# Kernel tuning notes

Measured on AMD Instinct MI355X. Metric: run time of the kernel, lower is better.

The kernel has to match this reference:

```python
import jax, jax.numpy as jnp
import numpy as np

N = 20000
NUM_FEATURES = 128
HIDDEN = 32
HEADS = 8
NUM_CLASSES = 40
NEG_SLOPE = 0.2  # PyG GATConv default


def setup_inputs() -> dict:
    key = jax.random.key(0)
    ks = jax.random.split(key, 10)
    E = 640000
    x = jax.random.normal(ks[0], (N, NUM_FEATURES), dtype=jnp.float32)
    edge_index = jax.random.randint(ks[1], (2, E), 0, N, dtype=jnp.int64)
    s1 = 1.0 / np.sqrt(NUM_FEATURES)
    s2 = 1.0 / np.sqrt(HIDDEN * HEADS)
    W1 = jax.random.normal(ks[2], (NUM_FEATURES, HEADS * HIDDEN), dtype=jnp.float32) * s1
    a1_src = jax.random.normal(ks[3], (HEADS, HIDDEN), dtype=jnp.float32) * s2
    a1_dst = jax.random.normal(ks[4], (HEADS, HIDDEN), dtype=jnp.float32) * s2
    b1 = jnp.zeros((HEADS * HIDDEN,), dtype=jnp.float32)
    W2 = jax.random.normal(ks[5], (HEADS * HIDDEN, NUM_CLASSES), dtype=jnp.float32) * s2
    a2_src = jax.random.normal(ks[6], (1, NUM_CLASSES), dtype=jnp.float32) * 0.1
    a2_dst = jax.random.normal(ks[7], (1, NUM_CLASSES), dtype=jnp.float32) * 0.1
    b2 = jnp.zeros((NUM_CLASSES,), dtype=jnp.float32)
    return {"x": x, "edge_index": edge_index, "W1": W1, "a1_src": a1_src,
            "a1_dst": a1_dst, "b1": b1, "W2": W2, "a2_src": a2_src,
            "a2_dst": a2_dst, "b2": b2}


def gat_conv(x, src, dst, W, a_src, a_dst, bias, heads, out_ch, concat):
    """PyG GATConv (eval mode, self-loops already appended to src/dst)."""
    n = x.shape[0]
    h = (x @ W).reshape(n, heads, out_ch)                     # [N,H,C]
    alpha_s = jnp.einsum('nhc,hc->nh', h, a_src)              # [N,H]
    alpha_d = jnp.einsum('nhc,hc->nh', h, a_dst)
    e = alpha_s[src] + alpha_d[dst]                           # [E,H]
    e = jax.nn.leaky_relu(e, NEG_SLOPE)
    # segment softmax over incoming edges of each destination node
    m = jax.ops.segment_max(e, dst, num_segments=n)           # [N,H]
    m = jax.lax.stop_gradient(m)
    ex = jnp.exp(e - m[dst])                                  # [E,H]
    denom = jax.ops.segment_sum(ex, dst, num_segments=n)      # [N,H]
    alpha = ex / denom[dst]                                   # [E,H]
    msg = alpha[:, :, None] * h[src]                          # [E,H,C]
    out = jax.ops.segment_sum(msg, dst, num_segments=n)       # [N,H,C]
    if concat:
        out = out.reshape(n, heads * out_ch)
    else:
        out = out.mean(axis=1)
    return out + bias


def reference(x, edge_index, W1, a1_src, a1_dst, b1, W2, a2_src, a2_dst, b2):
    loops = jnp.arange(N, dtype=edge_index.dtype)
    src = jnp.concatenate([edge_index[0], loops])
    dst = jnp.concatenate([edge_index[1], loops])
    h = gat_conv(x, src, dst, W1, a1_src, a1_dst, b1, HEADS, HIDDEN, True)
    h = jax.nn.elu(h)
    out = gat_conv(h, src, dst, W2, a2_src, a2_dst, b2, 1, NUM_CLASSES, False)
    return jax.nn.log_softmax(out, axis=1)
```

## Files before the change

kernel.cpp:

```cpp
#include <hip/hip_runtime.h>
#include <hip/hip_fp16.h>
#include <math.h>

#define N 20000
#define F 128
#define C1 256
#define HEADS 8
#define HID 32
#define NC 40
#define NCP 64
#define NEG 0.2f

#define BSHIFT 7
#define NB 157
#define HBLOCKS 256
#define HM (NB * HBLOCKS)

#define PREPW_BLOCKS 16
#define W2PW_BLOCKS 6

#define QS ((size_t)N * 64)

typedef _Float16 half8 __attribute__((ext_vector_type(8)));
typedef float f32x4 __attribute__((ext_vector_type(4)));

__device__ __forceinline__ int edge_stride(const int* ei) {
    return (ei[1] == 0 && ei[3] == 0 && ei[5] == 0 && ei[7] == 0 && ei[9] == 0) ? 2 : 1;
}

__device__ __forceinline__ float lrelu(float v) { return v > 0.f ? v : NEG * v; }

__global__ __launch_bounds__(256) void k_misc(
    const float* __restrict__ W1, _Float16* __restrict__ w1sw,
    const float* __restrict__ W2, _Float16* __restrict__ w2sw,
    const int* __restrict__ ei, int E, int* __restrict__ hist)
{
    const int b = blockIdx.x;
    const int tid = threadIdx.x;
    if (b < PREPW_BLOCKS) {
        const int slot = b * 256 + tid;
        const int lane = slot & 63;
        const int tile = slot >> 6;
        const int nt = tile & 15, ks = tile >> 4;
        const int n = nt * 16 + (lane & 15);
        const int k0 = ks * 32 + (lane >> 4) * 8;
        half8 tmp;
#pragma unroll
        for (int j = 0; j < 8; j++) tmp[j] = (_Float16)W1[(k0 + j) * C1 + n];
        *reinterpret_cast<half8*>(&w1sw[(size_t)slot * 8]) = tmp;
    } else if (b < PREPW_BLOCKS + W2PW_BLOCKS) {
        const int slot = (b - PREPW_BLOCKS) * 256 + tid;
        const int lane = slot & 63;
        const int f = slot >> 6;
        const int nt = f % 3, ks = f / 3;
        const int n = nt * 16 + (lane & 15);
        const int k0 = ks * 32 + (lane >> 4) * 8;
        half8 tmp;
#pragma unroll
        for (int j = 0; j < 8; j++)
            tmp[j] = (n < NC) ? (_Float16)W2[(k0 + j) * NC + n] : (_Float16)0.f;
        *reinterpret_cast<half8*>(&w2sw[(size_t)slot * 8]) = tmp;
    } else {
        __shared__ int hcnt[NB];
        const int hb = b - PREPW_BLOCKS - W2PW_BLOCKS;
        if (tid < NB) hcnt[tid] = 0;
        __syncthreads();
        const int ET = E + N;
        const int per = (ET + HBLOCKS - 1) / HBLOCKS;
        const int lo = hb * per;
        const int hi = (lo + per < ET) ? (lo + per) : ET;
        const int st = edge_stride(ei);
        for (int i = lo + tid; i < hi; i += 256) {
            const int d = (i < E) ? ei[(size_t)st * (E + i)] : (i - E);
            atomicAdd(&hcnt[d >> BSHIFT], 1);
        }
        __syncthreads();
        if (tid < NB) hist[tid * HBLOCKS + hb] = hcnt[tid];
    }
}

__global__ __launch_bounds__(256) void k_gemm1_mfma(
    const float* __restrict__ x, const _Float16* __restrict__ w1sw,
    const float* __restrict__ a1s, const float* __restrict__ a1d,
    __half* __restrict__ qh1,
    float* __restrict__ as1, float* __restrict__ ad1)
{
    const int lane = threadIdx.x & 63;
    const int wid = (blockIdx.x * 256 + threadIdx.x) >> 6;
    const int m0 = wid * 16;
    const int g = lane >> 4, lm = lane & 15;
    const int arow = m0 + lm;
    half8 a[4];
    if (arow < N) {
        const float* xr = x + (size_t)arow * F;
#pragma unroll
        for (int ks = 0; ks < 4; ks++) {
            const float4 v0 = *reinterpret_cast<const float4*>(&xr[ks * 32 + g * 8]);
            const float4 v1 = *reinterpret_cast<const float4*>(&xr[ks * 32 + g * 8 + 4]);
            half8 t;
            t[0] = (_Float16)v0.x; t[1] = (_Float16)v0.y; t[2] = (_Float16)v0.z; t[3] = (_Float16)v0.w;
            t[4] = (_Float16)v1.x; t[5] = (_Float16)v1.y; t[6] = (_Float16)v1.z; t[7] = (_Float16)v1.w;
            a[ks] = t;
        }
    } else {
#pragma unroll
        for (int ks = 0; ks < 4; ks++) {
            half8 t;
#pragma unroll
            for (int j = 0; j < 8; j++) t[j] = (_Float16)0.f;
            a[ks] = t;
        }
    }
    const int rbase = m0 + g * 4;
    float ps[4] = {0.f, 0.f, 0.f, 0.f}, pd[4] = {0.f, 0.f, 0.f, 0.f};
#pragma unroll
    for (int nt = 0; nt < 16; nt++) {
        f32x4 acc = {0.f, 0.f, 0.f, 0.f};
#pragma unroll
        for (int ks = 0; ks < 4; ks++) {
            const half8 bfr = *reinterpret_cast<const half8*>(&w1sw[(size_t)((ks * 16 + nt) * 64 + lane) * 8]);
            acc = __builtin_amdgcn_mfma_f32_16x16x32_f16(a[ks], bfr, acc, 0, 0, 0);
        }
        const int col = nt * 16 + lm;
        const int q = col >> 6, cq = col & 63;
        const float av = a1s[col], dv = a1d[col];
#pragma unroll
        for (int r = 0; r < 4; r++) {
            const int row = rbase + r;
            if (row < N) qh1[(size_t)q * QS + (size_t)row * 64 + cq] = __float2half((float)acc[r]);
            ps[r] = fmaf((float)acc[r], av, ps[r]);
            pd[r] = fmaf((float)acc[r], dv, pd[r]);
        }
        if (nt & 1) {
#pragma unroll
            for (int off = 1; off <= 8; off <<= 1) {
#pragma unroll
                for (int r = 0; r < 4; r++) {
                    ps[r] += __shfl_xor(ps[r], off);
                    pd[r] += __shfl_xor(pd[r], off);
                }
            }
            if (lm == 0) {
                const int head = nt >> 1;
#pragma unroll
                for (int r = 0; r < 4; r++) {
                    const int row = rbase + r;
                    if (row < N) {
                        as1[row * HEADS + head] = ps[r];
                        ad1[row * HEADS + head] = pd[r];
                    }
                }
            }
#pragma unroll
            for (int r = 0; r < 4; r++) { ps[r] = 0.f; pd[r] = 0.f; }
        }
    }
}

__global__ __launch_bounds__(256) void k_scatter2(
    const int* __restrict__ ei, int E, const int* __restrict__ hist,
    int* __restrict__ buck, int* __restrict__ bstart)
{
    __shared__ int cur[NB];
    __shared__ int bs[160];
    __shared__ int wbase[4];
    const int hb = blockIdx.x;
    const int tid = threadIdx.x;
    const int lane = tid & 63, wid = tid >> 6;
    int rp = 0;
    if (tid < NB) {
        const int4* hp = (const int4*)&hist[tid * HBLOCKS];
        int s = 0;
#pragma unroll 4
        for (int k = 0; k < 64; k++) {
            const int4 v = hp[k];
            s += (v.x + v.y) + (v.z + v.w);
            const int b4 = 4 * k;
            rp += ((b4 + 0) < hb ? v.x : 0) + ((b4 + 1) < hb ? v.y : 0)
                + ((b4 + 2) < hb ? v.z : 0) + ((b4 + 3) < hb ? v.w : 0);
        }
        bs[tid] = s;
    }
    __syncthreads();
    const int vin = (tid < NB) ? bs[tid] : 0;
    int v = vin;
#pragma unroll
    for (int off = 1; off < 64; off <<= 1) {
        const int u = __shfl_up(v, off, 64);
        if (lane >= off) v += u;
    }
    if (lane == 63) wbase[wid] = v;
    __syncthreads();
    if (tid < 64) {
        int w = (lane < 4) ? wbase[lane] : 0;
        const int orig = w;
#pragma unroll
        for (int off = 1; off < 4; off <<= 1) {
            const int u = __shfl_up(w, off, 64);
            if (lane >= off) w += u;
        }
        if (lane < 4) wbase[lane] = w - orig;
    }
    __syncthreads();
    if (tid < NB) {
        const int base = wbase[wid] + v - vin;
        cur[tid] = base + rp;
        if (hb == 0) bstart[tid] = base;
    }
    __syncthreads();
    const int ET = E + N;
    const int per = (ET + HBLOCKS - 1) / HBLOCKS;
    const int lo = hb * per;
    const int hi = (lo + per < ET) ? (lo + per) : ET;
    const int st = edge_stride(ei);
    for (int i = lo + tid; i < hi; i += 256) {
        int s, d;
        if (i < E) { s = ei[(size_t)st * i]; d = ei[(size_t)st * (E + i)]; }
        else       { s = i - E; d = i - E; }
        const int slot = atomicAdd(&cur[d >> BSHIFT], 1);
        buck[slot] = ((d & 127) << 16) | s;
    }
}

__global__ __launch_bounds__(256) void k_bucket(
    const int* __restrict__ bstart, const int* __restrict__ buck, int ET,
    int* __restrict__ csr, int* __restrict__ rowptr)
{
    __shared__ int cnt[128];
    __shared__ int pfx[128];
    const int b = blockIdx.x;
    const int tid = threadIdx.x;
    const int start = bstart[b];
    const int end = (b == NB - 1) ? ET : bstart[b + 1];
    if (tid < 128) cnt[tid] = 0;
    __syncthreads();
    for (int i = start + tid; i < end; i += 256)
        atomicAdd(&cnt[buck[i] >> 16], 1);
    __syncthreads();
    if (tid < 128) pfx[tid] = cnt[tid];
    __syncthreads();
    for (int off = 1; off < 128; off <<= 1) {
        int u = 0;
        if (tid < 128 && tid >= off) u = pfx[tid - off];
        __syncthreads();
        if (tid < 128) pfx[tid] += u;
        __syncthreads();
    }
    if (tid < 128) {
        const int node = b * 128 + tid;
        const int ebase = start + pfx[tid] - cnt[tid];
        if (node < N) rowptr[node] = ebase;
        cnt[tid] = ebase;
    }
    if (b == NB - 1 && tid == 0) rowptr[N] = ET;
    if (b == NB - 1 && tid < 64) csr[ET + tid] = 0;
    __syncthreads();
    for (int i = start + tid; i < end; i += 256) {
        const int val = buck[i];
        const int slot = atomicAdd(&cnt[val >> 16], 1);
        csr[slot] = val & 0xFFFF;
    }
}

__global__ __launch_bounds__(256) void k_agg1(
    const int* __restrict__ rowptr, const int* __restrict__ csr,
    const __half* __restrict__ qh1,
    const float* __restrict__ as1, const float* __restrict__ ad1,
    const float* __restrict__ b1, __half* __restrict__ h1p)
{
    __shared__ __align__(16) float wlds[8][2][36];
    __shared__ __align__(16) int slds[8][36];
    const int tid = threadIdx.x;
    const int l5 = tid & 31;
    const int sub = tid >> 5;
    const int hq = blockIdx.x & 3;
    const int n = (blockIdx.x >> 2) * 8 + sub;
    const int cq = l5 * 2;
    const int hsel = l5 >> 4;
    const float2 dv2 = *reinterpret_cast<const float2*>(&ad1[n * HEADS + hq * 2]);
    const int beg = rowptr[n], end = rowptr[n + 1];
    const __half* plane = qh1 + (size_t)hq * QS;
    float* w0 = wlds[sub][0];
    float* w1 = wlds[sub][1];
    const float* wc = wlds[sub][hsel];
    int* sl = slds[sub];
    float ax = 0.f, ay = 0.f, accw = 0.f;
    for (int cs = beg; cs < end; cs += 32) {
        const int m = end - cs;
        {
            const int s = csr[cs + l5];
            const float2 a2 = *reinterpret_cast<const float2*>(&as1[s * HEADS + hq * 2]);
            const bool ok = l5 < m;
            sl[l5] = s;
            w0[l5] = ok ? __expf(lrelu(a2.x + dv2.x)) : 0.f;
            w1[l5] = ok ? __expf(lrelu(a2.y + dv2.y)) : 0.f;
        }
        const int mm8 = (m < 32) ? ((m + 7) & ~7) : 32;
        for (int j0 = 0; j0 < mm8; j0 += 8) {
            const int4 sa = *reinterpret_cast<const int4*>(&sl[j0]);
            const int4 sb = *reinterpret_cast<const int4*>(&sl[j0 + 4]);
            const float4 wa = *reinterpret_cast<const float4*>(&wc[j0]);
            const float4 wb = *reinterpret_cast<const float4*>(&wc[j0 + 4]);
            const float2 gA = __half22float2(*reinterpret_cast<const __half2*>(&plane[(size_t)sa.x * 64 + cq]));
            const float2 gB = __half22float2(*reinterpret_cast<const __half2*>(&plane[(size_t)sa.y * 64 + cq]));
            const float2 gC = __half22float2(*reinterpret_cast<const __half2*>(&plane[(size_t)sa.z * 64 + cq]));
            const float2 gD = __half22float2(*reinterpret_cast<const __half2*>(&plane[(size_t)sa.w * 64 + cq]));
            const float2 gE = __half22float2(*reinterpret_cast<const __half2*>(&plane[(size_t)sb.x * 64 + cq]));
            const float2 gF = __half22float2(*reinterpret_cast<const __half2*>(&plane[(size_t)sb.y * 64 + cq]));
            const float2 gG = __half22float2(*reinterpret_cast<const __half2*>(&plane[(size_t)sb.z * 64 + cq]));
            const float2 gH = __half22float2(*reinterpret_cast<const __half2*>(&plane[(size_t)sb.w * 64 + cq]));
            accw += (wa.x + wa.y) + (wa.z + wa.w) + (wb.x + wb.y) + (wb.z + wb.w);
            ax = fmaf(wa.x, gA.x, ax); ay = fmaf(wa.x, gA.y, ay);
            ax = fmaf(wa.y, gB.x, ax); ay = fmaf(wa.y, gB.y, ay);
            ax = fmaf(wa.z, gC.x, ax); ay = fmaf(wa.z, gC.y, ay);
            ax = fmaf(wa.w, gD.x, ax); ay = fmaf(wa.w, gD.y, ay);
            ax = fmaf(wb.x, gE.x, ax); ay = fmaf(wb.x, gE.y, ay);
            ax = fmaf(wb.y, gF.x, ax); ay = fmaf(wb.y, gF.y, ay);
            ax = fmaf(wb.z, gG.x, ax); ay = fmaf(wb.z, gG.y, ay);
            ax = fmaf(wb.w, gH.x, ax); ay = fmaf(wb.w, gH.y, ay);
        }
    }
    const float inv = 1.f / accw;
    const int ch = hq * 64 + cq;
    float ox = ax * inv + b1[ch];
    float oy = ay * inv + b1[ch + 1];
    ox = (ox > 0.f) ? ox : (__expf(ox) - 1.f);
    oy = (oy > 0.f) ? oy : (__expf(oy) - 1.f);
    *reinterpret_cast<__half2*>(&h1p[(size_t)n * C1 + ch]) = __floats2half2_rn(ox, oy);
}

__global__ __launch_bounds__(256) void k_gemm2_mfma(
    const __half* __restrict__ h1p, const _Float16* __restrict__ w2sw,
    const float* __restrict__ a2s, const float* __restrict__ a2d,
    __half* __restrict__ h2h, float* __restrict__ as2, float* __restrict__ ad2)
{
    const int lane = threadIdx.x & 63;
    const int wid = (blockIdx.x * 256 + threadIdx.x) >> 6;
    const int m0 = wid * 16;
    const int g = lane >> 4, lm = lane & 15;
    const int arow = m0 + lm;
    half8 a[8];
    if (arow < N) {
        const __half* hr = h1p + (size_t)arow * C1;
#pragma unroll
        for (int ks = 0; ks < 8; ks++)
            a[ks] = *reinterpret_cast<const half8*>(&hr[ks * 32 + g * 8]);
    } else {
#pragma unroll
        for (int ks = 0; ks < 8; ks++) {
            half8 t;
#pragma unroll
            for (int j = 0; j < 8; j++) t[j] = (_Float16)0.f;
            a[ks] = t;
        }
    }
    f32x4 acc[3];
#pragma unroll
    for (int nt = 0; nt < 3; nt++) acc[nt] = (f32x4){0.f, 0.f, 0.f, 0.f};
#pragma unroll
    for (int ks = 0; ks < 8; ks++) {
#pragma unroll
        for (int nt = 0; nt < 3; nt++) {
            const half8 bfr = *reinterpret_cast<const half8*>(&w2sw[(size_t)((ks * 3 + nt) * 64 + lane) * 8]);
            acc[nt] = __builtin_amdgcn_mfma_f32_16x16x32_f16(a[ks], bfr, acc[nt], 0, 0, 0);
        }
    }
    const int rbase = m0 + g * 4;
    float av[3], dvv[3];
#pragma unroll
    for (int nt = 0; nt < 3; nt++) {
        const int col = nt * 16 + lm;
        av[nt]  = (col < NC) ? a2s[col] : 0.f;
        dvv[nt] = (col < NC) ? a2d[col] : 0.f;
    }
#pragma unroll
    for (int r = 0; r < 4; r++) {
        const int row = rbase + r;
        float ps = 0.f, pd = 0.f;
#pragma unroll
        for (int nt = 0; nt < 3; nt++) {
            const float v = (float)acc[nt][r];
            const int col = nt * 16 + lm;
            if (row < N && col < NC) h2h[(size_t)row * NCP + col] = __float2half(v);
            ps = fmaf(v, av[nt], ps);
            pd = fmaf(v, dvv[nt], pd);
        }
#pragma unroll
        for (int off = 1; off <= 8; off <<= 1) {
            ps += __shfl_xor(ps, off);
            pd += __shfl_xor(pd, off);
        }
        if (lm == 0 && row < N) { as2[row] = ps; ad2[row] = pd; }
    }
}

__global__ __launch_bounds__(256) void k_agg2(
    const int* __restrict__ rowptr, const int* __restrict__ csr,
    const __half* __restrict__ h2h, const float* __restrict__ as2,
    const float* __restrict__ ad2, const float* __restrict__ b2,
    float* __restrict__ out)
{
    __shared__ __align__(16) float wl[4][68];
    __shared__ __align__(16) int sl2[4][68];
    const int lane = threadIdx.x & 63;
    const int wv = threadIdx.x >> 6;
    const int n = (blockIdx.x * blockDim.x + threadIdx.x) >> 6;
    const int c = lane;
    const int cc = (c < NC) ? c : (NC - 1);
    const float adv = ad2[n];
    const int beg = rowptr[n], end = rowptr[n + 1];
    float* w = wl[wv];
    int* sl = sl2[wv];
    float acc = 0.f, accw = 0.f;
    for (int cs = beg; cs < end; cs += 64) {
        const int m = end - cs;
        {
            const int s = csr[cs + lane];
            sl[lane] = s;
            w[lane] = (lane < m) ? __expf(lrelu(as2[s] + adv)) : 0.f;
        }
        const int mm8 = (m < 64) ? ((m + 7) & ~7) : 64;
        for (int j0 = 0; j0 < mm8; j0 += 8) {
            const int4 sa = *reinterpret_cast<const int4*>(&sl[j0]);
            const int4 sb = *reinterpret_cast<const int4*>(&sl[j0 + 4]);
            const float4 wa = *reinterpret_cast<const float4*>(&w[j0]);
            const float4 wb = *reinterpret_cast<const float4*>(&w[j0 + 4]);
            const float g0 = __half2float(h2h[(size_t)sa.x * NCP + cc]);
            const float g1 = __half2float(h2h[(size_t)sa.y * NCP + cc]);
            const float g2 = __half2float(h2h[(size_t)sa.z * NCP + cc]);
            const float g3 = __half2float(h2h[(size_t)sa.w * NCP + cc]);
            const float g4 = __half2float(h2h[(size_t)sb.x * NCP + cc]);
            const float g5 = __half2float(h2h[(size_t)sb.y * NCP + cc]);
            const float g6 = __half2float(h2h[(size_t)sb.z * NCP + cc]);
            const float g7 = __half2float(h2h[(size_t)sb.w * NCP + cc]);
            accw += (wa.x + wa.y) + (wa.z + wa.w) + (wb.x + wb.y) + (wb.z + wb.w);
            acc = fmaf(wa.x, g0, acc);
            acc = fmaf(wa.y, g1, acc);
            acc = fmaf(wa.z, g2, acc);
            acc = fmaf(wa.w, g3, acc);
            acc = fmaf(wb.x, g4, acc);
            acc = fmaf(wb.y, g5, acc);
            acc = fmaf(wb.z, g6, acc);
            acc = fmaf(wb.w, g7, acc);
        }
    }
    const float v = acc / accw + b2[cc];
    float m = (c < NC) ? v : -1e30f;
#pragma unroll
    for (int off = 32; off >= 1; off >>= 1) m = fmaxf(m, __shfl_xor(m, off));
    float S = (c < NC) ? __expf(v - m) : 0.f;
#pragma unroll
    for (int off = 32; off >= 1; off >>= 1) S += __shfl_xor(S, off);
    if (c < NC) out[(size_t)n * NC + c] = v - m - logf(S);
}

extern "C" void kernel_launch(void* const* d_in, const int* in_sizes, int n_in,
                              void* d_out, int out_size, void* d_ws, size_t ws_size,
                              hipStream_t stream)
{
    const float* x   = (const float*)d_in[0];
    const int*   ei  = (const int*)d_in[1];
    const float* W1  = (const float*)d_in[2];
    const float* a1s = (const float*)d_in[3];
    const float* a1d = (const float*)d_in[4];
    const float* b1  = (const float*)d_in[5];
    const float* W2  = (const float*)d_in[6];
    const float* a2s = (const float*)d_in[7];
    const float* a2d = (const float*)d_in[8];
    const float* b2  = (const float*)d_in[9];
    float* out = (float*)d_out;

    const int E  = in_sizes[1] / 2;
    const int ET = E + N;

    auto align64 = [](size_t v) { return (v + 63) & ~(size_t)63; };
    char* ws = (char*)d_ws;
    size_t off = 0;
    _Float16* w1sw = (_Float16*)(ws + off); off = align64(off + (size_t)4096 * 8 * 2);
    _Float16* w2sw = (_Float16*)(ws + off); off = align64(off + (size_t)1536 * 8 * 2);
    __half* qh1 = (__half*)(ws + off); off = align64(off + (size_t)N * C1 * 2);
    __half* h1p = (__half*)(ws + off); off = align64(off + (size_t)N * C1 * 2);
    __half* h2h = (__half*)(ws + off); off = align64(off + (size_t)N * NCP * 2);
    float* as1 = (float*)(ws + off); off = align64(off + (size_t)N * HEADS * 4);
    float* ad1 = (float*)(ws + off); off = align64(off + (size_t)N * HEADS * 4);
    float* as2 = (float*)(ws + off); off = align64(off + (size_t)N * 4);
    float* ad2 = (float*)(ws + off); off = align64(off + (size_t)N * 4);
    int* hist   = (int*)(ws + off); off = align64(off + (size_t)HM * 4);
    int* bstart = (int*)(ws + off); off = align64(off + (size_t)NB * 4);
    int* buck   = (int*)(ws + off); off = align64(off + (size_t)ET * 4);
    int* rowptr = (int*)(ws + off); off = align64(off + (size_t)(N + 1) * 4);
    int* csr    = (int*)(ws + off); off = align64(off + (size_t)ET * 4 + 256);

    k_misc<<<PREPW_BLOCKS + W2PW_BLOCKS + HBLOCKS, 256, 0, stream>>>(W1, w1sw, W2, w2sw, ei, E, hist);
    k_gemm1_mfma<<<313, 256, 0, stream>>>(x, w1sw, a1s, a1d, qh1, as1, ad1);
    k_scatter2<<<HBLOCKS, 256, 0, stream>>>(ei, E, hist, buck, bstart);
    k_bucket<<<NB, 256, 0, stream>>>(bstart, buck, ET, csr, rowptr);
    k_agg1<<<N / 2, 256, 0, stream>>>(rowptr, csr, qh1, as1, ad1, b1, h1p);
    k_gemm2_mfma<<<313, 256, 0, stream>>>(h1p, w2sw, a2s, a2d, h2h, as2, ad2);
    k_agg2<<<5000, 256, 0, stream>>>(rowptr, csr, h2h, as2, ad2, b2, out);
}
```

Measured before the change: 183.4 us.

## Split GEMM1 columns across waves, persistent agg1 grid, prefetch next edge chunk

GEMM1 now gives each wave half of the 16 output column tiles, doubling the grid to 626 blocks for more parallelism. The agg1 kernel switches from one block per 8 nodes to a fixed 2048-block grid-stride loop, and both aggregation kernels prefetch the next chunk's source indices and attention scores while the current chunk is processed. The aim is to hide gather latency and cut launch and tail costs. In exchange, each GEMM1 wave reloads the full A fragment to do half the work, and the persistent loop may balance load less evenly.

```diff
diff --git a/kernel.cpp b/kernel.cpp
--- a/kernel.cpp
+++ b/kernel.cpp
@@ -20,6 +20,7 @@
 #define W2PW_BLOCKS 6
 
 #define QS ((size_t)N * 64)
+#define AGG1_BLOCKS 2048
 
 typedef _Float16 half8 __attribute__((ext_vector_type(8)));
 typedef float f32x4 __attribute__((ext_vector_type(4)));
@@ -87,7 +88,9 @@
 {
     const int lane = threadIdx.x & 63;
     const int wid = (blockIdx.x * 256 + threadIdx.x) >> 6;
-    const int m0 = wid * 16;
+    const int tile = wid >> 1;
+    const int hs = wid & 1;
+    const int m0 = tile * 16;
     const int g = lane >> 4, lm = lane & 15;
     const int arow = m0 + lm;
     half8 a[4];
@@ -114,7 +117,8 @@
     const int rbase = m0 + g * 4;
     float ps[4] = {0.f, 0.f, 0.f, 0.f}, pd[4] = {0.f, 0.f, 0.f, 0.f};
 #pragma unroll
-    for (int nt = 0; nt < 16; nt++) {
+    for (int ntl = 0; ntl < 8; ntl++) {
+        const int nt = hs * 8 + ntl;
         f32x4 acc = {0.f, 0.f, 0.f, 0.f};
 #pragma unroll
         for (int ks = 0; ks < 4; ks++) {
@@ -131,7 +135,7 @@
             ps[r] = fmaf((float)acc[r], av, ps[r]);
             pd[r] = fmaf((float)acc[r], dv, pd[r]);
         }
-        if (nt & 1) {
+        if (ntl & 1) {
 #pragma unroll
             for (int off = 1; off <= 8; off <<= 1) {
 #pragma unroll
@@ -141,7 +145,7 @@
                 }
             }
             if (lm == 0) {
-                const int head = nt >> 1;
+                const int head = hs * 4 + (ntl >> 1);
 #pragma unroll
                 for (int r = 0; r < 4; r++) {
                     const int row = rbase + r;
@@ -274,59 +278,67 @@
     const int l5 = tid & 31;
     const int sub = tid >> 5;
     const int hq = blockIdx.x & 3;
-    const int n = (blockIdx.x >> 2) * 8 + sub;
+    const int slotsPerQ = (gridDim.x >> 2) * 8;
+    const int slot0 = (blockIdx.x >> 2) * 8 + sub;
     const int cq = l5 * 2;
     const int hsel = l5 >> 4;
-    const float2 dv2 = *reinterpret_cast<const float2*>(&ad1[n * HEADS + hq * 2]);
-    const int beg = rowptr[n], end = rowptr[n + 1];
     const __half* plane = qh1 + (size_t)hq * QS;
     float* w0 = wlds[sub][0];
     float* w1 = wlds[sub][1];
     const float* wc = wlds[sub][hsel];
     int* sl = slds[sub];
-    float ax = 0.f, ay = 0.f, accw = 0.f;
-    for (int cs = beg; cs < end; cs += 32) {
-        const int m = end - cs;
-        {
-            const int s = csr[cs + l5];
-            const float2 a2 = *reinterpret_cast<const float2*>(&as1[s * HEADS + hq * 2]);
-            const bool ok = l5 < m;
-            sl[l5] = s;
-            w0[l5] = ok ? __expf(lrelu(a2.x + dv2.x)) : 0.f;
-            w1[l5] = ok ? __expf(lrelu(a2.y + dv2.y)) : 0.f;
-        }
-        const int mm8 = (m < 32) ? ((m + 7) & ~7) : 32;
-        for (int j0 = 0; j0 < mm8; j0 += 8) {
-            const int4 sa = *reinterpret_cast<const int4*>(&sl[j0]);
-            const int4 sb = *reinterpret_cast<const int4*>(&sl[j0 + 4]);
-            const float4 wa = *reinterpret_cast<const float4*>(&wc[j0]);
-            const float4 wb = *reinterpret_cast<const float4*>(&wc[j0 + 4]);
-            const float2 gA = __half22float2(*reinterpret_cast<const __half2*>(&plane[(size_t)sa.x * 64 + cq]));
-            const float2 gB = __half22float2(*reinterpret_cast<const __half2*>(&plane[(size_t)sa.y * 64 + cq]));
-            const float2 gC = __half22float2(*reinterpret_cast<const __half2*>(&plane[(size_t)sa.z * 64 + cq]));
-            const float2 gD = __half22float2(*reinterpret_cast<const __half2*>(&plane[(size_t)sa.w * 64 + cq]));
-            const float2 gE = __half22float2(*reinterpret_cast<const __half2*>(&plane[(size_t)sb.x * 64 + cq]));
-            const float2 gF = __half22float2(*reinterpret_cast<const __half2*>(&plane[(size_t)sb.y * 64 + cq]));
-            const float2 gG = __half22float2(*reinterpret_cast<const __half2*>(&plane[(size_t)sb.z * 64 + cq]));
-            const float2 gH = __half22float2(*reinterpret_cast<const __half2*>(&plane[(size_t)sb.w * 64 + cq]));
-            accw += (wa.x + wa.y) + (wa.z + wa.w) + (wb.x + wb.y) + (wb.z + wb.w);
-            ax = fmaf(wa.x, gA.x, ax); ay = fmaf(wa.x, gA.y, ay);
-            ax = fmaf(wa.y, gB.x, ax); ay = fmaf(wa.y, gB.y, ay);
-            ax = fmaf(wa.z, gC.x, ax); ay = fmaf(wa.z, gC.y, ay);
-            ax = fmaf(wa.w, gD.x, ax); ay = fmaf(wa.w, gD.y, ay);
-            ax = fmaf(wb.x, gE.x, ax); ay = fmaf(wb.x, gE.y, ay);
-            ax = fmaf(wb.y, gF.x, ax); ay = fmaf(wb.y, gF.y, ay);
-            ax = fmaf(wb.z, gG.x, ax); ay = fmaf(wb.z, gG.y, ay);
-            ax = fmaf(wb.w, gH.x, ax); ay = fmaf(wb.w, gH.y, ay);
-        }
-    }
-    const float inv = 1.f / accw;
     const int ch = hq * 64 + cq;
-    float ox = ax * inv + b1[ch];
-    float oy = ay * inv + b1[ch + 1];
-    ox = (ox > 0.f) ? ox : (__expf(ox) - 1.f);
-    oy = (oy > 0.f) ? oy : (__expf(oy) - 1.f);
-    *reinterpret_cast<__half2*>(&h1p[(size_t)n * C1 + ch]) = __floats2half2_rn(ox, oy);
+    const float bx = b1[ch], by = b1[ch + 1];
+    for (int n = slot0; n < N; n += slotsPerQ) {
+        const float2 dv2 = *reinterpret_cast<const float2*>(&ad1[n * HEADS + hq * 2]);
+        const int beg = rowptr[n], end = rowptr[n + 1];
+        float ax = 0.f, ay = 0.f, accw = 0.f;
+        int s_pf = csr[beg + l5];
+        float2 a_pf = *reinterpret_cast<const float2*>(&as1[s_pf * HEADS + hq * 2]);
+        for (int cs = beg; cs < end; cs += 32) {
+            const int m = end - cs;
+            {
+                const bool ok = l5 < m;
+                sl[l5] = s_pf;
+                w0[l5] = ok ? __expf(lrelu(a_pf.x + dv2.x)) : 0.f;
+                w1[l5] = ok ? __expf(lrelu(a_pf.y + dv2.y)) : 0.f;
+            }
+            if (cs + 32 < end) {
+                s_pf = csr[cs + 32 + l5];
+                a_pf = *reinterpret_cast<const float2*>(&as1[s_pf * HEADS + hq * 2]);
+            }
+            const int mm8 = (m < 32) ? ((m + 7) & ~7) : 32;
+            for (int j0 = 0; j0 < mm8; j0 += 8) {
+                const int4 sa = *reinterpret_cast<const int4*>(&sl[j0]);
+                const int4 sb = *reinterpret_cast<const int4*>(&sl[j0 + 4]);
+                const float4 wa = *reinterpret_cast<const float4*>(&wc[j0]);
+                const float4 wb = *reinterpret_cast<const float4*>(&wc[j0 + 4]);
+                const float2 gA = __half22float2(*reinterpret_cast<const __half2*>(&plane[(size_t)sa.x * 64 + cq]));
+                const float2 gB = __half22float2(*reinterpret_cast<const __half2*>(&plane[(size_t)sa.y * 64 + cq]));
+                const float2 gC = __half22float2(*reinterpret_cast<const __half2*>(&plane[(size_t)sa.z * 64 + cq]));
+                const float2 gD = __half22float2(*reinterpret_cast<const __half2*>(&plane[(size_t)sa.w * 64 + cq]));
+                const float2 gE = __half22float2(*reinterpret_cast<const __half2*>(&plane[(size_t)sb.x * 64 + cq]));
+                const float2 gF = __half22float2(*reinterpret_cast<const __half2*>(&plane[(size_t)sb.y * 64 + cq]));
+                const float2 gG = __half22float2(*reinterpret_cast<const __half2*>(&plane[(size_t)sb.z * 64 + cq]));
+                const float2 gH = __half22float2(*reinterpret_cast<const __half2*>(&plane[(size_t)sb.w * 64 + cq]));
+                accw += (wa.x + wa.y) + (wa.z + wa.w) + (wb.x + wb.y) + (wb.z + wb.w);
+                ax = fmaf(wa.x, gA.x, ax); ay = fmaf(wa.x, gA.y, ay);
+                ax = fmaf(wa.y, gB.x, ax); ay = fmaf(wa.y, gB.y, ay);
+                ax = fmaf(wa.z, gC.x, ax); ay = fmaf(wa.z, gC.y, ay);
+                ax = fmaf(wa.w, gD.x, ax); ay = fmaf(wa.w, gD.y, ay);
+                ax = fmaf(wb.x, gE.x, ax); ay = fmaf(wb.x, gE.y, ay);
+                ax = fmaf(wb.y, gF.x, ax); ay = fmaf(wb.y, gF.y, ay);
+                ax = fmaf(wb.z, gG.x, ax); ay = fmaf(wb.z, gG.y, ay);
+                ax = fmaf(wb.w, gH.x, ax); ay = fmaf(wb.w, gH.y, ay);
+            }
+        }
+        const float inv = 1.f / accw;
+        float ox = ax * inv + bx;
+        float oy = ay * inv + by;
+        ox = (ox > 0.f) ? ox : (__expf(ox) - 1.f);
+        oy = (oy > 0.f) ? oy : (__expf(oy) - 1.f);
+        *reinterpret_cast<__half2*>(&h1p[(size_t)n * C1 + ch]) = __floats2half2_rn(ox, oy);
+    }
 }
 
 __global__ __launch_bounds__(256) void k_gemm2_mfma(
@@ -412,12 +424,17 @@
     float* w = wl[wv];
     int* sl = sl2[wv];
     float acc = 0.f, accw = 0.f;
+    int s_pf = csr[beg + lane];
+    float a_pf = as2[s_pf];
     for (int cs = beg; cs < end; cs += 64) {
         const int m = end - cs;
         {
-            const int s = csr[cs + lane];
-            sl[lane] = s;
-            w[lane] = (lane < m) ? __expf(lrelu(as2[s] + adv)) : 0.f;
+            sl[lane] = s_pf;
+            w[lane] = (lane < m) ? __expf(lrelu(a_pf + adv)) : 0.f;
+        }
+        if (cs + 64 < end) {
+            s_pf = csr[cs + 64 + lane];
+            a_pf = as2[s_pf];
         }
         const int mm8 = (m < 64) ? ((m + 7) & ~7) : 64;
         for (int j0 = 0; j0 < mm8; j0 += 8) {
@@ -492,10 +509,10 @@
     int* csr    = (int*)(ws + off); off = align64(off + (size_t)ET * 4 + 256);
 
     k_misc<<<PREPW_BLOCKS + W2PW_BLOCKS + HBLOCKS, 256, 0, stream>>>(W1, w1sw, W2, w2sw, ei, E, hist);
-    k_gemm1_mfma<<<313, 256, 0, stream>>>(x, w1sw, a1s, a1d, qh1, as1, ad1);
+    k_gemm1_mfma<<<626, 256, 0, stream>>>(x, w1sw, a1s, a1d, qh1, as1, ad1);
     k_scatter2<<<HBLOCKS, 256, 0, stream>>>(ei, E, hist, buck, bstart);
     k_bucket<<<NB, 256, 0, stream>>>(bstart, buck, ET, csr, rowptr);
-    k_agg1<<<N / 2, 256, 0, stream>>>(rowptr, csr, qh1, as1, ad1, b1, h1p);
+    k_agg1<<<AGG1_BLOCKS, 256, 0, stream>>>(rowptr, csr, qh1, as1, ad1, b1, h1p);
     k_gemm2_mfma<<<313, 256, 0, stream>>>(h1p, w2sw, a2s, a2d, h2h, as2, ad2);
     k_agg2<<<5000, 256, 0, stream>>>(rowptr, csr, h2h, as2, ad2, b2, out);
 }
```

After: 182.9 us. Within noise of the previous version (-0.3%).

## Fuse GEMM1 with edge scatter and prefetch and pre-shift gather offsets in aggregation

Applied to the files above, without the earlier changes.

Merges the layer-1 MFMA GEMM and the edge-bucket scatter into one launch. Block ranges pick the role, and each GEMM wave now covers half the output columns for a 16-row tile, which doubles the GEMM block count. The aggregation kernels store source indices pre-shifted to byte offsets and use 32-bit unsigned address arithmetic for the gathers. agg2 also prefetches the next chunk of CSR indices and attention scores. The aim is to remove one launch, overlap independent work, and cut address-math and load latency, at the cost of more A-row reloads in the GEMM.

```diff
diff --git a/kernel.cpp b/kernel.cpp
--- a/kernel.cpp
+++ b/kernel.cpp
@@ -20,6 +20,7 @@
 #define W2PW_BLOCKS 6
 
 #define QS ((size_t)N * 64)
+#define G1_BLOCKS 626
 
 typedef _Float16 half8 __attribute__((ext_vector_type(8)));
 typedef float f32x4 __attribute__((ext_vector_type(4)));
@@ -79,146 +80,147 @@
     }
 }
 
-__global__ __launch_bounds__(256) void k_gemm1_mfma(
+__global__ __launch_bounds__(256) void k_fused1(
     const float* __restrict__ x, const _Float16* __restrict__ w1sw,
     const float* __restrict__ a1s, const float* __restrict__ a1d,
-    __half* __restrict__ qh1,
-    float* __restrict__ as1, float* __restrict__ ad1)
-{
-    const int lane = threadIdx.x & 63;
-    const int wid = (blockIdx.x * 256 + threadIdx.x) >> 6;
-    const int m0 = wid * 16;
-    const int g = lane >> 4, lm = lane & 15;
-    const int arow = m0 + lm;
-    half8 a[4];
-    if (arow < N) {
-        const float* xr = x + (size_t)arow * F;
-#pragma unroll
-        for (int ks = 0; ks < 4; ks++) {
-            const float4 v0 = *reinterpret_cast<const float4*>(&xr[ks * 32 + g * 8]);
-            const float4 v1 = *reinterpret_cast<const float4*>(&xr[ks * 32 + g * 8 + 4]);
-            half8 t;
-            t[0] = (_Float16)v0.x; t[1] = (_Float16)v0.y; t[2] = (_Float16)v0.z; t[3] = (_Float16)v0.w;
-            t[4] = (_Float16)v1.x; t[5] = (_Float16)v1.y; t[6] = (_Float16)v1.z; t[7] = (_Float16)v1.w;
-            a[ks] = t;
+    __half* __restrict__ qh1, float* __restrict__ as1, float* __restrict__ ad1,
+    const int* __restrict__ ei, int E, const int* __restrict__ hist,
+    int* __restrict__ buck, int* __restrict__ bstart)
+{
+    const int tid = threadIdx.x;
+    if (blockIdx.x < HBLOCKS) {
+        __shared__ int cur[NB];
+        __shared__ int bs[160];
+        __shared__ int wbase[4];
+        const int hb = blockIdx.x;
+        const int lane = tid & 63, wid = tid >> 6;
+        int rp = 0;
+        if (tid < NB) {
+            const int4* hp = (const int4*)&hist[tid * HBLOCKS];
+            int s = 0;
+#pragma unroll 4
+            for (int k = 0; k < 64; k++) {
+                const int4 v = hp[k];
+                s += (v.x + v.y) + (v.z + v.w);
+                const int b4 = 4 * k;
+                rp += ((b4 + 0) < hb ? v.x : 0) + ((b4 + 1) < hb ? v.y : 0)
+                    + ((b4 + 2) < hb ? v.z : 0) + ((b4 + 3) < hb ? v.w : 0);
+            }
+            bs[tid] = s;
+        }
+        __syncthreads();
+        const int vin = (tid < NB) ? bs[tid] : 0;
+        int v = vin;
+#pragma unroll
+        for (int off = 1; off < 64; off <<= 1) {
+            const int u = __shfl_up(v, off, 64);
+            if (lane >= off) v += u;
+        }
+        if (lane == 63) wbase[wid] = v;
+        __syncthreads();
+        if (tid < 64) {
+            int w = (lane < 4) ? wbase[lane] : 0;
+            const int orig = w;
+#pragma unroll
+            for (int off = 1; off < 4; off <<= 1) {
+                const int u = __shfl_up(w, off, 64);
+                if (lane >= off) w += u;
+            }
+            if (lane < 4) wbase[lane] = w - orig;
+        }
+        __syncthreads();
+        if (tid < NB) {
+            const int base = wbase[wid] + v - vin;
+            cur[tid] = base + rp;
+            if (hb == 0) bstart[tid] = base;
+        }
+        __syncthreads();
+        const int ET = E + N;
+        const int per = (ET + HBLOCKS - 1) / HBLOCKS;
+        const int lo = hb * per;
+        const int hi = (lo + per < ET) ? (lo + per) : ET;
+        const int st = edge_stride(ei);
+        for (int i = lo + tid; i < hi; i += 256) {
+            int s, d;
+            if (i < E) { s = ei[(size_t)st * i]; d = ei[(size_t)st * (E + i)]; }
+            else       { s = i - E; d = i - E; }
+            const int slot = atomicAdd(&cur[d >> BSHIFT], 1);
+            buck[slot] = ((d & 127) << 16) | s;
         }
     } else {
-#pragma unroll
-        for (int ks = 0; ks < 4; ks++) {
-            half8 t;
-#pragma unroll
-            for (int j = 0; j < 8; j++) t[j] = (_Float16)0.f;
-            a[ks] = t;
-        }
-    }
-    const int rbase = m0 + g * 4;
-    float ps[4] = {0.f, 0.f, 0.f, 0.f}, pd[4] = {0.f, 0.f, 0.f, 0.f};
-#pragma unroll
-    for (int nt = 0; nt < 16; nt++) {
-        f32x4 acc = {0.f, 0.f, 0.f, 0.f};
-#pragma unroll
-        for (int ks = 0; ks < 4; ks++) {
-            const half8 bfr = *reinterpret_cast<const half8*>(&w1sw[(size_t)((ks * 16 + nt) * 64 + lane) * 8]);
-            acc = __builtin_amdgcn_mfma_f32_16x16x32_f16(a[ks], bfr, acc, 0, 0, 0);
-        }
-        const int col = nt * 16 + lm;
-        const int q = col >> 6, cq = col & 63;
-        const float av = a1s[col], dv = a1d[col];
-#pragma unroll
-        for (int r = 0; r < 4; r++) {
-            const int row = rbase + r;
-            if (row < N) qh1[(size_t)q * QS + (size_t)row * 64 + cq] = __float2half((float)acc[r]);
-            ps[r] = fmaf((float)acc[r], av, ps[r]);
-            pd[r] = fmaf((float)acc[r], dv, pd[r]);
-        }
-        if (nt & 1) {
-#pragma unroll
-            for (int off = 1; off <= 8; off <<= 1) {
-#pragma unroll
-                for (int r = 0; r < 4; r++) {
-                    ps[r] += __shfl_xor(ps[r], off);
-                    pd[r] += __shfl_xor(pd[r], off);
-                }
-            }
-            if (lm == 0) {
-                const int head = nt >> 1;
-#pragma unroll
-                for (int r = 0; r < 4; r++) {
-                    const int row = rbase + r;
-                    if (row < N) {
-                        as1[row * HEADS + head] = ps[r];
-                        ad1[row * HEADS + head] = pd[r];
+        const int lane = tid & 63;
+        const int wid = ((blockIdx.x - HBLOCKS) * 256 + tid) >> 6;
+        const int tile = wid >> 1;
+        const int hs = wid & 1;
+        const int m0 = tile * 16;
+        const int g = lane >> 4, lm = lane & 15;
+        const int arow = m0 + lm;
+        half8 a[4];
+        if (arow < N) {
+            const float* xr = x + (size_t)arow * F;
+#pragma unroll
+            for (int ks = 0; ks < 4; ks++) {
+                const float4 v0 = *reinterpret_cast<const float4*>(&xr[ks * 32 + g * 8]);
+                const float4 v1 = *reinterpret_cast<const float4*>(&xr[ks * 32 + g * 8 + 4]);
+                half8 t;
+                t[0] = (_Float16)v0.x; t[1] = (_Float16)v0.y; t[2] = (_Float16)v0.z; t[3] = (_Float16)v0.w;
+                t[4] = (_Float16)v1.x; t[5] = (_Float16)v1.y; t[6] = (_Float16)v1.z; t[7] = (_Float16)v1.w;
+                a[ks] = t;
+            }
+        } else {
+#pragma unroll
+            for (int ks = 0; ks < 4; ks++) {
+                half8 t;
+#pragma unroll
+                for (int j = 0; j < 8; j++) t[j] = (_Float16)0.f;
+                a[ks] = t;
+            }
+        }
+        const int rbase = m0 + g * 4;
+        float ps[4] = {0.f, 0.f, 0.f, 0.f}, pd[4] = {0.f, 0.f, 0.f, 0.f};
+#pragma unroll
+        for (int ntl = 0; ntl < 8; ntl++) {
+            const int nt = hs * 8 + ntl;
+            f32x4 acc = {0.f, 0.f, 0.f, 0.f};
+#pragma unroll
+            for (int ks = 0; ks < 4; ks++) {
+                const half8 bfr = *reinterpret_cast<const half8*>(&w1sw[(size_t)((ks * 16 + nt) * 64 + lane) * 8]);
+                acc = __builtin_amdgcn_mfma_f32_16x16x32_f16(a[ks], bfr, acc, 0, 0, 0);
+            }
+            const int col = nt * 16 + lm;
+            const int q = col >> 6, cq = col & 63;
+            const float av = a1s[col], dv = a1d[col];
+#pragma unroll
+            for (int r = 0; r < 4; r++) {
+                const int row = rbase + r;
+                if (row < N) qh1[(size_t)q * QS + (size_t)row * 64 + cq] = __float2half((float)acc[r]);
+                ps[r] = fmaf((float)acc[r], av, ps[r]);
+                pd[r] = fmaf((float)acc[r], dv, pd[r]);
+            }
+            if (ntl & 1) {
+#pragma unroll
+                for (int off = 1; off <= 8; off <<= 1) {
+#pragma unroll
+                    for (int r = 0; r < 4; r++) {
+                        ps[r] += __shfl_xor(ps[r], off);
+                        pd[r] += __shfl_xor(pd[r], off);
                     }
                 }
-            }
-#pragma unroll
-            for (int r = 0; r < 4; r++) { ps[r] = 0.f; pd[r] = 0.f; }
-        }
-    }
-}
-
-__global__ __launch_bounds__(256) void k_scatter2(
-    const int* __restrict__ ei, int E, const int* __restrict__ hist,
-    int* __restrict__ buck, int* __restrict__ bstart)
-{
-    __shared__ int cur[NB];
-    __shared__ int bs[160];
-    __shared__ int wbase[4];
-    const int hb = blockIdx.x;
-    const int tid = threadIdx.x;
-    const int lane = tid & 63, wid = tid >> 6;
-    int rp = 0;
-    if (tid < NB) {
-        const int4* hp = (const int4*)&hist[tid * HBLOCKS];
-        int s = 0;
-#pragma unroll 4
-        for (int k = 0; k < 64; k++) {
-            const int4 v = hp[k];
-            s += (v.x + v.y) + (v.z + v.w);
-            const int b4 = 4 * k;
-            rp += ((b4 + 0) < hb ? v.x : 0) + ((b4 + 1) < hb ? v.y : 0)
-                + ((b4 + 2) < hb ? v.z : 0) + ((b4 + 3) < hb ? v.w : 0);
-        }
-        bs[tid] = s;
-    }
-    __syncthreads();
-    const int vin = (tid < NB) ? bs[tid] : 0;
-    int v = vin;
-#pragma unroll
-    for (int off = 1; off < 64; off <<= 1) {
-        const int u = __shfl_up(v, off, 64);
-        if (lane >= off) v += u;
-    }
-    if (lane == 63) wbase[wid] = v;
-    __syncthreads();
-    if (tid < 64) {
-        int w = (lane < 4) ? wbase[lane] : 0;
-        const int orig = w;
-#pragma unroll
-        for (int off = 1; off < 4; off <<= 1) {
-            const int u = __shfl_up(w, off, 64);
-            if (lane >= off) w += u;
-        }
-        if (lane < 4) wbase[lane] = w - orig;
-    }
-    __syncthreads();
-    if (tid < NB) {
-        const int base = wbase[wid] + v - vin;
-        cur[tid] = base + rp;
-        if (hb == 0) bstart[tid] = base;
-    }
-    __syncthreads();
-    const int ET = E + N;
-    const int per = (ET + HBLOCKS - 1) / HBLOCKS;
-    const int lo = hb * per;
-    const int hi = (lo + per < ET) ? (lo + per) : ET;
-    const int st = edge_stride(ei);
-    for (int i = lo + tid; i < hi; i += 256) {
-        int s, d;
-        if (i < E) { s = ei[(size_t)st * i]; d = ei[(size_t)st * (E + i)]; }
-        else       { s = i - E; d = i - E; }
-        const int slot = atomicAdd(&cur[d >> BSHIFT], 1);
-        buck[slot] = ((d & 127) << 16) | s;
+                if (lm == 0) {
+                    const int head = hs * 4 + (ntl >> 1);
+#pragma unroll
+                    for (int r = 0; r < 4; r++) {
+                        const int row = rbase + r;
+                        if (row < N) {
+                            as1[row * HEADS + head] = ps[r];
+                            ad1[row * HEADS + head] = pd[r];
+                        }
+                    }
+                }
+#pragma unroll
+                for (int r = 0; r < 4; r++) { ps[r] = 0.f; pd[r] = 0.f; }
+            }
+        }
     }
 }
 
@@ -276,10 +278,11 @@
     const int hq = blockIdx.x & 3;
     const int n = (blockIdx.x >> 2) * 8 + sub;
     const int cq = l5 * 2;
+    const int lob = l5 * 4;
     const int hsel = l5 >> 4;
     const float2 dv2 = *reinterpret_cast<const float2*>(&ad1[n * HEADS + hq * 2]);
     const int beg = rowptr[n], end = rowptr[n + 1];
-    const __half* plane = qh1 + (size_t)hq * QS;
+    const char* planeb = (const char*)(qh1 + (size_t)hq * QS);
     float* w0 = wlds[sub][0];
     float* w1 = wlds[sub][1];
     const float* wc = wlds[sub][hsel];
@@ -291,7 +294,7 @@
             const int s = csr[cs + l5];
             const float2 a2 = *reinterpret_cast<const float2*>(&as1[s * HEADS + hq * 2]);
             const bool ok = l5 < m;
-            sl[l5] = s;
+            sl[l5] = s << 7;
             w0[l5] = ok ? __expf(lrelu(a2.x + dv2.x)) : 0.f;
             w1[l5] = ok ? __expf(lrelu(a2.y + dv2.y)) : 0.f;
         }
@@ -301,14 +304,14 @@
             const int4 sb = *reinterpret_cast<const int4*>(&sl[j0 + 4]);
             const float4 wa = *reinterpret_cast<const float4*>(&wc[j0]);
             const float4 wb = *reinterpret_cast<const float4*>(&wc[j0 + 4]);
-            const float2 gA = __half22float2(*reinterpret_cast<const __half2*>(&plane[(size_t)sa.x * 64 + cq]));
-            const float2 gB = __half22float2(*reinterpret_cast<const __half2*>(&plane[(size_t)sa.y * 64 + cq]));
-            const float2 gC = __half22float2(*reinterpret_cast<const __half2*>(&plane[(size_t)sa.z * 64 + cq]));
-            const float2 gD = __half22float2(*reinterpret_cast<const __half2*>(&plane[(size_t)sa.w * 64 + cq]));
-            const float2 gE = __half22float2(*reinterpret_cast<const __half2*>(&plane[(size_t)sb.x * 64 + cq]));
-            const float2 gF = __half22float2(*reinterpret_cast<const __half2*>(&plane[(size_t)sb.y * 64 + cq]));
-            const float2 gG = __half22float2(*reinterpret_cast<const __half2*>(&plane[(size_t)sb.z * 64 + cq]));
-            const float2 gH = __half22float2(*reinterpret_cast<const __half2*>(&plane[(size_t)sb.w * 64 + cq]));
+            const float2 gA = __half22float2(*(const __half2*)(planeb + (unsigned)(sa.x + lob)));
+            const float2 gB = __half22float2(*(const __half2*)(planeb + (unsigned)(sa.y + lob)));
+            const float2 gC = __half22float2(*(const __half2*)(planeb + (unsigned)(sa.z + lob)));
+            const float2 gD = __half22float2(*(const __half2*)(planeb + (unsigned)(sa.w + lob)));
+            const float2 gE = __half22float2(*(const __half2*)(planeb + (unsigned)(sb.x + lob)));
+            const float2 gF = __half22float2(*(const __half2*)(planeb + (unsigned)(sb.y + lob)));
+            const float2 gG = __half22float2(*(const __half2*)(planeb + (unsigned)(sb.z + lob)));
+            const float2 gH = __half22float2(*(const __half2*)(planeb + (unsigned)(sb.w + lob)));
             accw += (wa.x + wa.y) + (wa.z + wa.w) + (wb.x + wb.y) + (wb.z + wb.w);
             ax = fmaf(wa.x, gA.x, ax); ay = fmaf(wa.x, gA.y, ay);
             ax = fmaf(wa.y, gB.x, ax); ay = fmaf(wa.y, gB.y, ay);
@@ -407,17 +410,24 @@
     const int n = (blockIdx.x * blockDim.x + threadIdx.x) >> 6;
     const int c = lane;
     const int cc = (c < NC) ? c : (NC - 1);
+    const int lob = cc * 2;
     const float adv = ad2[n];
     const int beg = rowptr[n], end = rowptr[n + 1];
+    const char* h2b = (const char*)h2h;
     float* w = wl[wv];
     int* sl = sl2[wv];
     float acc = 0.f, accw = 0.f;
+    int s_pf = csr[beg + lane];
+    float a_pf = as2[s_pf];
     for (int cs = beg; cs < end; cs += 64) {
         const int m = end - cs;
         {
-            const int s = csr[cs + lane];
-            sl[lane] = s;
-            w[lane] = (lane < m) ? __expf(lrelu(as2[s] + adv)) : 0.f;
+            sl[lane] = s_pf << 7;
+            w[lane] = (lane < m) ? __expf(lrelu(a_pf + adv)) : 0.f;
+        }
+        if (cs + 64 < end) {
+            s_pf = csr[cs + 64 + lane];
+            a_pf = as2[s_pf];
         }
         const int mm8 = (m < 64) ? ((m + 7) & ~7) : 64;
         for (int j0 = 0; j0 < mm8; j0 += 8) {
@@ -425,14 +435,14 @@
             const int4 sb = *reinterpret_cast<const int4*>(&sl[j0 + 4]);
             const float4 wa = *reinterpret_cast<const float4*>(&w[j0]);
             const float4 wb = *reinterpret_cast<const float4*>(&w[j0 + 4]);
-            const float g0 = __half2float(h2h[(size_t)sa.x * NCP + cc]);
-            const float g1 = __half2float(h2h[(size_t)sa.y * NCP + cc]);
-            const float g2 = __half2float(h2h[(size_t)sa.z * NCP + cc]);
-            const float g3 = __half2float(h2h[(size_t)sa.w * NCP + cc]);
-            const float g4 = __half2float(h2h[(size_t)sb.x * NCP + cc]);
-            const float g5 = __half2float(h2h[(size_t)sb.y * NCP + cc]);
-            const float g6 = __half2float(h2h[(size_t)sb.z * NCP + cc]);
-            const float g7 = __half2float(h2h[(size_t)sb.w * NCP + cc]);
+            const float g0 = __half2float(*(const __half*)(h2b + (unsigned)(sa.x + lob)));
+            const float g1 = __half2float(*(const __half*)(h2b + (unsigned)(sa.y + lob)));
+            const float g2 = __half2float(*(const __half*)(h2b + (unsigned)(sa.z + lob)));
+            const float g3 = __half2float(*(const __half*)(h2b + (unsigned)(sa.w + lob)));
+            const float g4 = __half2float(*(const __half*)(h2b + (unsigned)(sb.x + lob)));
+            const float g5 = __half2float(*(const __half*)(h2b + (unsigned)(sb.y + lob)));
+            const float g6 = __half2float(*(const __half*)(h2b + (unsigned)(sb.z + lob)));
+            const float g7 = __half2float(*(const __half*)(h2b + (unsigned)(sb.w + lob)));
             accw += (wa.x + wa.y) + (wa.z + wa.w) + (wb.x + wb.y) + (wb.z + wb.w);
             acc = fmaf(wa.x, g0, acc);
             acc = fmaf(wa.y, g1, acc);
@@ -492,8 +502,8 @@
     int* csr    = (int*)(ws + off); off = align64(off + (size_t)ET * 4 + 256);
 
     k_misc<<<PREPW_BLOCKS + W2PW_BLOCKS + HBLOCKS, 256, 0, stream>>>(W1, w1sw, W2, w2sw, ei, E, hist);
-    k_gemm1_mfma<<<313, 256, 0, stream>>>(x, w1sw, a1s, a1d, qh1, as1, ad1);
-    k_scatter2<<<HBLOCKS, 256, 0, stream>>>(ei, E, hist, buck, bstart);
+    k_fused1<<<HBLOCKS + G1_BLOCKS, 256, 0, stream>>>(x, w1sw, a1s, a1d, qh1, as1, ad1,
+                                                      ei, E, hist, buck, bstart);
     k_bucket<<<NB, 256, 0, stream>>>(bstart, buck, ET, csr, rowptr);
     k_agg1<<<N / 2, 256, 0, stream>>>(rowptr, csr, qh1, as1, ad1, b1, h1p);
     k_gemm2_mfma<<<313, 256, 0, stream>>>(h1p, w2sw, a2s, a2d, h2h, as2, ad2);
```

New measurement: 166.4 us (median of 2 runs). 9.3% less time.
